# Optimization experiments

Measured on AMD Instinct MI355X. Metric: run time of the kernel, lower is better.

The kernel has to match this reference:

```python
import jax, jax.numpy as jnp
import numpy as np

N_NODES = 50000
N_EDGES = 800000
IN_DIM = 128
HID = 8
HEADS = 8
OUT_DIM = 64
NEG_SLOPE = 0.2


def setup_inputs() -> dict:
    key = jax.random.key(0)
    ks = jax.random.split(key, 8)
    x = jax.random.normal(ks[0], (N_NODES, IN_DIM), dtype=jnp.float32)
    edge_index = jax.random.randint(ks[1], (2, N_EDGES), 0, N_NODES, dtype=jnp.int64)
    W1 = jax.random.normal(ks[2], (IN_DIM, HEADS * HID), dtype=jnp.float32) / np.sqrt(IN_DIM)
    a_src1 = jax.random.normal(ks[3], (HEADS, HID), dtype=jnp.float32)
    a_dst1 = jax.random.normal(ks[4], (HEADS, HID), dtype=jnp.float32)
    b1 = jnp.zeros((HEADS * HID,), dtype=jnp.float32)
    W2 = jax.random.normal(ks[5], (HEADS * HID, OUT_DIM), dtype=jnp.float32) / np.sqrt(HEADS * HID)
    a_src2 = jax.random.normal(ks[6], (1, OUT_DIM), dtype=jnp.float32)
    a_dst2 = jax.random.normal(ks[7], (1, OUT_DIM), dtype=jnp.float32)
    b2 = jnp.zeros((OUT_DIM,), dtype=jnp.float32)
    return {"x": x, "edge_index": edge_index, "W1": W1, "a_src1": a_src1,
            "a_dst1": a_dst1, "b1": b1, "W2": W2, "a_src2": a_src2,
            "a_dst2": a_dst2, "b2": b2}


def gat_conv(x, src, dst, W, a_src, a_dst, b, heads, ch):
    # PyG GATConv (eval mode): linear -> per-edge LeakyReLU score ->
    # segment-softmax over incoming edges -> weighted scatter-add -> +bias
    n = x.shape[0]
    h = (x @ W).reshape(n, heads, ch)               # [N,H,C]
    score_src = jnp.einsum('nhc,hc->nh', h, a_src)  # [N,H]
    score_dst = jnp.einsum('nhc,hc->nh', h, a_dst)  # [N,H]
    e = jax.nn.leaky_relu(score_src[src] + score_dst[dst], NEG_SLOPE)  # [E,H]
    m = jax.ops.segment_max(e, dst, num_segments=n)
    m = jnp.where(jnp.isfinite(m), m, 0.0)
    p = jnp.exp(e - m[dst])
    denom = jax.ops.segment_sum(p, dst, num_segments=n)
    alpha = p / (denom[dst] + 1e-16)                # [E,H]
    out = jax.ops.segment_sum(h[src] * alpha[:, :, None], dst, num_segments=n)
    return out.reshape(n, heads * ch) + b


def reference(x, edge_index, W1, a_src1, a_dst1, b1, W2, a_src2, a_dst2, b2):
    n = x.shape[0]
    # add_self_loops=True (PyG default)
    loops = jnp.arange(n, dtype=edge_index.dtype)
    src = jnp.concatenate([edge_index[0], loops])
    dst = jnp.concatenate([edge_index[1], loops])
    h = gat_conv(x, src, dst, W1, a_src1, a_dst1, b1, HEADS, HID)
    h = jax.nn.elu(h)
    out = gat_conv(h, src, dst, W2, a_src2, a_dst2, b2, 1, OUT_DIM)
    return out
```

## Files before the change

kernel.cpp:

```cpp
#include <hip/hip_runtime.h>
#include <hip/hip_fp16.h>
#include <math.h>

#define N_NODES 50000
#define N_EDGES 800000
#define ET (N_EDGES + N_NODES)
#define IN_DIM 128
#define H1DIM 64
#define HEADS 8
#define HID 8
#define OUT_DIM 64
#define NEG_SLOPE 0.2f

#define SCAN_TILE 256
#define NTILES ((N_NODES + SCAN_TILE - 1) / SCAN_TILE)
#define RC 8
#define PF 6

#define LIN1_WAVES (N_NODES / 8)
#define LIN1_BLOCKS ((LIN1_WAVES + 3) / 4)
#define EB ((ET + 255) / 256)

__device__ __forceinline__ float lrelu(float v) { return v >= 0.f ? v : NEG_SLOPE * v; }

__device__ __forceinline__ float rdlane(float v, int l) {
    return __int_as_float(__builtin_amdgcn_readlane(__float_as_int(v), l));
}

__device__ __forceinline__ int xcc_id() {
    int v;
    asm volatile("s_getreg_b32 %0, hwreg(HW_REG_XCC_ID)" : "=s"(v));
    return v & 7;
}

__device__ __forceinline__ void fma8raw(uint4 u, float alpha, float* a) {
    float2 f0 = __half22float2(*(const __half2*)&u.x);
    float2 f1 = __half22float2(*(const __half2*)&u.y);
    float2 f2 = __half22float2(*(const __half2*)&u.z);
    float2 f3 = __half22float2(*(const __half2*)&u.w);
    a[0] += f0.x * alpha; a[1] += f0.y * alpha;
    a[2] += f1.x * alpha; a[3] += f1.y * alpha;
    a[4] += f2.x * alpha; a[5] += f2.y * alpha;
    a[6] += f3.x * alpha; a[7] += f3.y * alpha;
}

__device__ __forceinline__ void fma8h(const __half* __restrict__ base, float alpha, float* a) {
    fma8raw(*reinterpret_cast<const uint4*>(base), alpha, a);
}

__device__ __forceinline__ void edge_nodes(const int* __restrict__ ei, int e, int& s, int& d) {
    if (e < N_EDGES) { s = ei[e]; d = ei[N_EDGES + e]; }
    else             { s = e - N_EDGES; d = s; }
}


__global__ __launch_bounds__(256) void cl1_kernel(
    const int* __restrict__ ei, int* __restrict__ cnt8, int* __restrict__ pos,
    const float* __restrict__ x, const float* __restrict__ W1,
    const float* __restrict__ a_src, const float* __restrict__ a_dst,
    __half* __restrict__ h1, float* __restrict__ ssrc, float* __restrict__ sdst)
{
    if (blockIdx.x >= LIN1_BLOCKS) {
        int i = (blockIdx.x - LIN1_BLOCKS) * 256 + threadIdx.x;
        if (i >= ET) return;
        int s, d; edge_nodes(ei, i, s, d);
        int c = xcc_id();
        int r = atomicAdd(&cnt8[c * N_NODES + d], 1);
        pos[i] = r | (c << 28);
        return;
    }
    int wid = threadIdx.x >> 6, t = threadIdx.x & 63;
    int g = blockIdx.x * 4 + wid;
    if (g >= LIN1_WAVES) return;
    int n0 = g * 8;

    float x0[8], x1[8];
    #pragma unroll
    for (int nn = 0; nn < 8; ++nn) {
        x0[nn] = x[(n0 + nn) * IN_DIM + t];
        x1[nn] = x[(n0 + nn) * IN_DIM + 64 + t];
    }
    float acc[8] = {0,0,0,0,0,0,0,0};
    #pragma unroll 8
    for (int k = 0; k < 64; ++k) {
        float w = W1[k * 64 + t];
        #pragma unroll
        for (int nn = 0; nn < 8; ++nn) acc[nn] += rdlane(x0[nn], k) * w;
    }
    #pragma unroll 8
    for (int k = 0; k < 64; ++k) {
        float w = W1[(k + 64) * 64 + t];
        #pragma unroll
        for (int nn = 0; nn < 8; ++nn) acc[nn] += rdlane(x1[nn], k) * w;
    }

    float av = a_src[t], bv = a_dst[t];
    #pragma unroll
    for (int nn = 0; nn < 8; ++nn) {
        int n = n0 + nn;
        h1[n * 64 + t] = __float2half(acc[nn]);
        float rs = acc[nn] * av, rd = acc[nn] * bv;
        rs += __shfl_xor(rs, 1); rs += __shfl_xor(rs, 2); rs += __shfl_xor(rs, 4);
        rd += __shfl_xor(rd, 1); rd += __shfl_xor(rd, 2); rd += __shfl_xor(rd, 4);
        if ((t & 7) == 0) { ssrc[n * 8 + (t >> 3)] = rs; sdst[n * 8 + (t >> 3)] = rd; }
    }
}


__global__ __launch_bounds__(SCAN_TILE) void scanA_kernel(
    const int* __restrict__ cnt8, int* __restrict__ row, int* __restrict__ aux)
{
    __shared__ int sh[SCAN_TILE];
    int t = threadIdx.x, i = blockIdx.x * SCAN_TILE + t;
    int v = 0;
    if (i < N_NODES) {
        #pragma unroll
        for (int c = 0; c < 8; ++c) v += cnt8[c * N_NODES + i];
    }
    sh[t] = v;
    __syncthreads();
    #pragma unroll
    for (int off = 1; off < SCAN_TILE; off <<= 1) {
        int add = (t >= off) ? sh[t - off] : 0;
        __syncthreads();
        sh[t] += add;
        __syncthreads();
    }
    if (i < N_NODES) row[i] = sh[t] - v;
    if (t == SCAN_TILE - 1) aux[blockIdx.x] = sh[t];
}

__global__ __launch_bounds__(SCAN_TILE) void scanB_kernel(int* __restrict__ aux, int* __restrict__ row) {
    __shared__ int sh[SCAN_TILE];
    int t = threadIdx.x;
    int v = (t < NTILES) ? aux[t] : 0;
    sh[t] = v;
    __syncthreads();
    #pragma unroll
    for (int off = 1; off < SCAN_TILE; off <<= 1) {
        int add = (t >= off) ? sh[t - off] : 0;
        __syncthreads();
        sh[t] += add;
        __syncthreads();
    }
    if (t < NTILES) aux[t] = sh[t] - v;
    if (t == NTILES - 1) row[N_NODES] = sh[t];
}

__global__ __launch_bounds__(SCAN_TILE) void scanC_kernel(
    const int* __restrict__ aux, int* __restrict__ row,
    const int* __restrict__ cnt8, int* __restrict__ off8)
{
    int i = blockIdx.x * SCAN_TILE + threadIdx.x;
    if (i >= N_NODES) return;
    int r = row[i] + aux[i >> 8];
    row[i] = r;
    int run = r;
    #pragma unroll
    for (int c = 0; c < 8; ++c) {
        off8[c * N_NODES + i] = run;
        run += cnt8[c * N_NODES + i];
    }
}

__global__ void fill_kernel(const int* __restrict__ ei, const int* __restrict__ off8,
                            const int* __restrict__ pos, int* __restrict__ adj)
{
    int i = blockIdx.x * blockDim.x + threadIdx.x;
    if (i >= ET) return;
    int s, d; edge_nodes(ei, i, s, d);
    int pr = pos[i];
    int c = (unsigned)pr >> 28;
    int r = pr & 0x0FFFFFFF;
    adj[off8[c * N_NODES + d] + r] = s;
}


__global__ __launch_bounds__(256) void l1_kernel(
    const int* __restrict__ row, const int* __restrict__ adj,
    const __half* __restrict__ h1, const float* __restrict__ s1, const float* __restrict__ t1,
    const float* __restrict__ b1, const float* __restrict__ W2,
    const float* __restrict__ as2, const float* __restrict__ ad2,
    __half* __restrict__ h2, float* __restrict__ s2, float* __restrict__ t2)
{
    int wid = threadIdx.x >> 6, t = threadIdx.x & 63;
    int half = t >> 5, tt = t & 31;
    int n = blockIdx.x * 8 + wid * 2 + half;
    int beg = row[n], end = row[n + 1];
    int slot = tt >> 3, h = tt & 7;
    float sd = t1[n * 8 + h];
    const int e0 = beg + slot;
    const int hb = half << 5;

    int   sv[RC];
    float p[RC];
    uint4 raw[PF];
    float m = -3e38f;
    #pragma unroll
    for (int it = 0; it < RC; ++it) {
        int e = e0 + it * 4;
        bool ok = e < end;
        int s = ok ? adj[e] : n;
        sv[it] = s;
        float v = ok ? lrelu(s1[s * 8 + h] + sd) : -3e38f;
        p[it] = v;
        m = fmaxf(m, v);
        if (it < PF) raw[it] = *reinterpret_cast<const uint4*>(h1 + (size_t)s * 64 + h * 8);
    }
    for (int e = e0 + RC * 4; e < end; e += 4)
        m = fmaxf(m, lrelu(s1[adj[e] * 8 + h] + sd));
    m = fmaxf(m, __shfl_xor(m, 8));
    m = fmaxf(m, __shfl_xor(m, 16));

    float den = 0.f;
    #pragma unroll
    for (int it = 0; it < RC; ++it) {
        float pe = __expf(p[it] - m);
        p[it] = pe;
        den += pe;
    }
    for (int e = e0 + RC * 4; e < end; e += 4)
        den += __expf(lrelu(s1[adj[e] * 8 + h] + sd) - m);
    den += __shfl_xor(den, 8);
    den += __shfl_xor(den, 16);
    float inv = 1.f / (den + 1e-16f);

    float a[8] = {0,0,0,0,0,0,0,0};
    #pragma unroll
    for (int it = 0; it < PF; ++it) fma8raw(raw[it], p[it] * inv, a);
    #pragma unroll
    for (int it = PF; it < RC; ++it) {
        int e = e0 + it * 4;
        if (e < end) fma8h(h1 + (size_t)sv[it] * 64 + h * 8, p[it] * inv, a);
    }
    for (int e = e0 + RC * 4; e < end; e += 4) {
        int s = adj[e];
        float alpha = __expf(lrelu(s1[s * 8 + h] + sd) - m) * inv;
        fma8h(h1 + (size_t)s * 64 + h * 8, alpha, a);
    }
    #pragma unroll
    for (int j = 0; j < 8; ++j) {
        a[j] += __shfl_xor(a[j], 8);
        a[j] += __shfl_xor(a[j], 16);
    }

    float ha0 = 0.f, ha1 = 0.f;
    int srcA = hb + (tt >> 3);
    #pragma unroll
    for (int j = 0; j < 8; ++j) {
        float vA = __shfl(a[j], srcA);
        float vB = __shfl(a[j], srcA + 4);
        if ((tt & 7) == j) { ha0 = vA; ha1 = vB; }
    }

    ha0 += b1[tt];
    ha1 += b1[tt + 32];
    ha0 = ha0 > 0.f ? ha0 : (__expf(ha0) - 1.f);
    ha1 = ha1 > 0.f ? ha1 : (__expf(ha1) - 1.f);

    float c0 = 0.f, c1 = 0.f;
    #pragma unroll 8
    for (int k = 0; k < 32; ++k) {
        float w = __shfl(ha0, hb + k);
        c0 += w * W2[k * 64 + tt];
        c1 += w * W2[k * 64 + tt + 32];
    }
    #pragma unroll 8
    for (int k = 0; k < 32; ++k) {
        float w = __shfl(ha1, hb + k);
        c0 += w * W2[(k + 32) * 64 + tt];
        c1 += w * W2[(k + 32) * 64 + tt + 32];
    }
    h2[n * 64 + tt]      = __float2half(c0);
    h2[n * 64 + tt + 32] = __float2half(c1);

    float rs = c0 * as2[tt] + c1 * as2[tt + 32];
    float rd = c0 * ad2[tt] + c1 * ad2[tt + 32];
    #pragma unroll
    for (int mk = 16; mk >= 1; mk >>= 1) {
        rs += __shfl_xor(rs, mk);
        rd += __shfl_xor(rd, mk);
    }
    if (tt == 0) { s2[n] = rs; t2[n] = rd; }
}


__global__ __launch_bounds__(256) void l2_kernel(
    const int* __restrict__ row, const int* __restrict__ adj,
    const __half* __restrict__ h2, const float* __restrict__ s2, const float* __restrict__ t2,
    const float* __restrict__ b2, float* __restrict__ out)
{
    int wid = threadIdx.x >> 6, t = threadIdx.x & 63;
    int half = t >> 5, tt = t & 31;
    int n = blockIdx.x * 8 + wid * 2 + half;
    int beg = row[n], end = row[n + 1];
    int slot = tt >> 3, g = tt & 7;
    float sd = t2[n];
    const int e0 = beg + slot;

    int   sv[RC];
    float p[RC];
    uint4 raw[PF];
    float m = -3e38f;
    #pragma unroll
    for (int it = 0; it < RC; ++it) {
        int e = e0 + it * 4;
        bool ok = e < end;
        int s = ok ? adj[e] : n;
        sv[it] = s;
        float v = ok ? lrelu(s2[s] + sd) : -3e38f;
        p[it] = v;
        m = fmaxf(m, v);
        if (it < PF) raw[it] = *reinterpret_cast<const uint4*>(h2 + (size_t)s * 64 + g * 8);
    }
    for (int e = e0 + RC * 4; e < end; e += 4)
        m = fmaxf(m, lrelu(s2[adj[e]] + sd));
    m = fmaxf(m, __shfl_xor(m, 8));
    m = fmaxf(m, __shfl_xor(m, 16));

    float den = 0.f;
    #pragma unroll
    for (int it = 0; it < RC; ++it) {
        float pe = __expf(p[it] - m);
        p[it] = pe;
        den += pe;
    }
    for (int e = e0 + RC * 4; e < end; e += 4)
        den += __expf(lrelu(s2[adj[e]] + sd) - m);
    den += __shfl_xor(den, 8);
    den += __shfl_xor(den, 16);
    float inv = 1.f / (den + 1e-16f);

    float a[8] = {0,0,0,0,0,0,0,0};
    #pragma unroll
    for (int it = 0; it < PF; ++it) fma8raw(raw[it], p[it] * inv, a);
    #pragma unroll
    for (int it = PF; it < RC; ++it) {
        int e = e0 + it * 4;
        if (e < end) fma8h(h2 + (size_t)sv[it] * 64 + g * 8, p[it] * inv, a);
    }
    for (int e = e0 + RC * 4; e < end; e += 4) {
        int s = adj[e];
        float alpha = __expf(lrelu(s2[s] + sd) - m) * inv;
        fma8h(h2 + (size_t)s * 64 + g * 8, alpha, a);
    }
    #pragma unroll
    for (int j = 0; j < 8; ++j) {
        a[j] += __shfl_xor(a[j], 8);
        a[j] += __shfl_xor(a[j], 16);
    }
    if (slot == 0) {
        float4 o0 = make_float4(a[0] + b2[g * 8 + 0], a[1] + b2[g * 8 + 1],
                                a[2] + b2[g * 8 + 2], a[3] + b2[g * 8 + 3]);
        float4 o1 = make_float4(a[4] + b2[g * 8 + 4], a[5] + b2[g * 8 + 5],
                                a[6] + b2[g * 8 + 6], a[7] + b2[g * 8 + 7]);
        float4* op = (float4*)(out + (size_t)n * 64 + g * 8);
        op[0] = o0; op[1] = o1;
    }
}

extern "C" void kernel_launch(void* const* d_in, const int* in_sizes, int n_in,
                              void* d_out, int out_size, void* d_ws, size_t ws_size,
                              hipStream_t stream)
{
    const float* x   = (const float*)d_in[0];
    const int* ei    = (const int*)d_in[1];
    const float* W1  = (const float*)d_in[2];
    const float* as1 = (const float*)d_in[3];
    const float* ad1 = (const float*)d_in[4];
    const float* b1  = (const float*)d_in[5];
    const float* W2  = (const float*)d_in[6];
    const float* as2 = (const float*)d_in[7];
    const float* ad2 = (const float*)d_in[8];
    const float* b2  = (const float*)d_in[9];
    float* out = (float*)d_out;

    char* wsb = (char*)d_ws;
    __half* h1  = (__half*)wsb;
    __half* h2  = h1 + (size_t)N_NODES * 64;
    float*  s1  = (float*)(h2 + (size_t)N_NODES * 64);
    float*  t1  = s1 + N_NODES * 8;
    float*  s2  = t1 + N_NODES * 8;
    float*  t2  = s2 + N_NODES;
    int*    cnt8 = (int*)(t2 + N_NODES);
    int*    off8 = cnt8 + 8 * N_NODES;
    int*    rowp = off8 + 8 * N_NODES;
    int*    aux  = rowp + N_NODES + 1;
    int*    adj  = aux + NTILES;
    int*    pos  = adj + ET;

    hipMemsetAsync(cnt8, 0, 8 * N_NODES * sizeof(int), stream);

    cl1_kernel<<<LIN1_BLOCKS + EB, 256, 0, stream>>>(ei, cnt8, pos, x, W1, as1, ad1, h1, s1, t1);

    scanA_kernel<<<NTILES, SCAN_TILE, 0, stream>>>(cnt8, rowp, aux);
    scanB_kernel<<<1, SCAN_TILE, 0, stream>>>(aux, rowp);
    scanC_kernel<<<NTILES, SCAN_TILE, 0, stream>>>(aux, rowp, cnt8, off8);
    fill_kernel<<<EB, 256, 0, stream>>>(ei, off8, pos, adj);

    l1_kernel<<<N_NODES / 8, 256, 0, stream>>>(rowp, adj, h1, s1, t1,
                                               b1, W2, as2, ad2, h2, s2, t2);

    l2_kernel<<<N_NODES / 8, 256, 0, stream>>>(rowp, adj, h2, s2, t2, b2, out);
}
```

Baseline: 232.9 us.

## Compute layer-1 linear projection with split-fp16 MFMA instead of readlane FMAs

The x@W1 projection moves from scalar readlane-broadcast FMAs to 16x16x32 f16 MFMA instructions. Each wave now handles 16 nodes instead of 8. x and W1 are each split into high and low fp16 parts, and three MFMAs per tile keep accuracy close to fp32. Every block stages the whole W1 split into shared memory, which adds a per-block LDS fill and 32KB of LDS use. The aim is to cut the VALU cost of the dense matmul stage.

Result: faster. 221.4 us (-4.9%).

```diff
diff --git a/kernel.cpp b/kernel.cpp
--- a/kernel.cpp
+++ b/kernel.cpp
@@ -17,15 +17,14 @@
 #define RC 8
 #define PF 6
 
-#define LIN1_WAVES (N_NODES / 8)
+#define LIN1_WAVES (N_NODES / 16)
 #define LIN1_BLOCKS ((LIN1_WAVES + 3) / 4)
 #define EB ((ET + 255) / 256)
 
+typedef _Float16 half8 __attribute__((ext_vector_type(8)));
+typedef float f32x4 __attribute__((ext_vector_type(4)));
+
 __device__ __forceinline__ float lrelu(float v) { return v >= 0.f ? v : NEG_SLOPE * v; }
-
-__device__ __forceinline__ float rdlane(float v, int l) {
-    return __int_as_float(__builtin_amdgcn_readlane(__float_as_int(v), l));
-}
 
 __device__ __forceinline__ int xcc_id() {
     int v;
@@ -69,40 +68,80 @@
         pos[i] = r | (c << 28);
         return;
     }
-    int wid = threadIdx.x >> 6, t = threadIdx.x & 63;
+
+    __shared__ __half bH[16 * 512];
+    __shared__ __half bL[16 * 512];
+
+    int tid = threadIdx.x;
+    #pragma unroll
+    for (int i = 0; i < 32; ++i) {
+        int idx = i * 256 + tid;
+        int f = idx >> 9, rr = idx & 511;
+        int l = rr >> 3, j = rr & 7;
+        int ks = f >> 2, ct = f & 3;
+        int k = ks * 32 + ((l >> 4) << 3) + j;
+        int c = (ct << 4) + (l & 15);
+        float w = W1[k * 64 + c];
+        __half hi = __float2half(w);
+        bH[idx] = hi;
+        bL[idx] = __float2half(w - __half2float(hi));
+    }
+    __syncthreads();
+
+    int wid = tid >> 6, t = tid & 63;
     int g = blockIdx.x * 4 + wid;
     if (g >= LIN1_WAVES) return;
-    int n0 = g * 8;
-
-    float x0[8], x1[8];
-    #pragma unroll
-    for (int nn = 0; nn < 8; ++nn) {
-        x0[nn] = x[(n0 + nn) * IN_DIM + t];
-        x1[nn] = x[(n0 + nn) * IN_DIM + 64 + t];
-    }
-    float acc[8] = {0,0,0,0,0,0,0,0};
-    #pragma unroll 8
-    for (int k = 0; k < 64; ++k) {
-        float w = W1[k * 64 + t];
+    int n0 = g * 16;
+    int row = t & 15, kq = t >> 4;
+
+    f32x4 acc[4] = {};
+    const float* xp = x + (size_t)(n0 + row) * IN_DIM + kq * 8;
+    #pragma unroll
+    for (int ks = 0; ks < 4; ++ks) {
+        float4 u0 = *reinterpret_cast<const float4*>(xp + ks * 32);
+        float4 u1 = *reinterpret_cast<const float4*>(xp + ks * 32 + 4);
+        float xv[8] = {u0.x, u0.y, u0.z, u0.w, u1.x, u1.y, u1.z, u1.w};
+        half8 ah, al;
         #pragma unroll
-        for (int nn = 0; nn < 8; ++nn) acc[nn] += rdlane(x0[nn], k) * w;
-    }
-    #pragma unroll 8
-    for (int k = 0; k < 64; ++k) {
-        float w = W1[(k + 64) * 64 + t];
+        for (int j = 0; j < 8; ++j) {
+            _Float16 h = (_Float16)xv[j];
+            ah[j] = h;
+            al[j] = (_Float16)(xv[j] - (float)h);
+        }
         #pragma unroll
-        for (int nn = 0; nn < 8; ++nn) acc[nn] += rdlane(x1[nn], k) * w;
-    }
-
-    float av = a_src[t], bv = a_dst[t];
-    #pragma unroll
-    for (int nn = 0; nn < 8; ++nn) {
-        int n = n0 + nn;
-        h1[n * 64 + t] = __float2half(acc[nn]);
-        float rs = acc[nn] * av, rd = acc[nn] * bv;
-        rs += __shfl_xor(rs, 1); rs += __shfl_xor(rs, 2); rs += __shfl_xor(rs, 4);
-        rd += __shfl_xor(rd, 1); rd += __shfl_xor(rd, 2); rd += __shfl_xor(rd, 4);
-        if ((t & 7) == 0) { ssrc[n * 8 + (t >> 3)] = rs; sdst[n * 8 + (t >> 3)] = rd; }
+        for (int ct = 0; ct < 4; ++ct) {
+            int f = ks * 4 + ct;
+            half8 bh = *reinterpret_cast<const half8*>(&bH[f * 512 + t * 8]);
+            half8 bl = *reinterpret_cast<const half8*>(&bL[f * 512 + t * 8]);
+            acc[ct] = __builtin_amdgcn_mfma_f32_16x16x32_f16(ah, bh, acc[ct], 0, 0, 0);
+            acc[ct] = __builtin_amdgcn_mfma_f32_16x16x32_f16(al, bh, acc[ct], 0, 0, 0);
+            acc[ct] = __builtin_amdgcn_mfma_f32_16x16x32_f16(ah, bl, acc[ct], 0, 0, 0);
+        }
+    }
+
+    float asv[4], adv[4];
+    #pragma unroll
+    for (int ct = 0; ct < 4; ++ct) {
+        asv[ct] = a_src[ct * 16 + (t & 15)];
+        adv[ct] = a_dst[ct * 16 + (t & 15)];
+    }
+    int rbase = n0 + (t >> 4) * 4;
+    #pragma unroll
+    for (int r = 0; r < 4; ++r) {
+        int n = rbase + r;
+        #pragma unroll
+        for (int ct = 0; ct < 4; ++ct) {
+            float v = acc[ct][r];
+            h1[(size_t)n * 64 + ct * 16 + (t & 15)] = __float2half(v);
+            float ps = v * asv[ct], pd = v * adv[ct];
+            ps += __shfl_xor(ps, 1); ps += __shfl_xor(ps, 2); ps += __shfl_xor(ps, 4);
+            pd += __shfl_xor(pd, 1); pd += __shfl_xor(pd, 2); pd += __shfl_xor(pd, 4);
+            if ((t & 7) == 0) {
+                int hd = ct * 2 + ((t >> 3) & 1);
+                ssrc[n * 8 + hd] = ps;
+                sdst[n * 8 + hd] = pd;
+            }
+        }
     }
 }
 
```
